# Kernel optimization log

Measured on AMD Instinct MI355X. Metric: run time of the kernel, lower is better.

The kernel has to match this reference:

```python
import jax, jax.numpy as jnp
import numpy as np

NUM_CLASSES = 80
INPUT_SHAPE = (416.0, 416.0)
ANCHORS_MASK0 = np.array([6, 7, 8])
CONF_THRES = 0.5
NMS_THRES = 0.4
IMAGE_SHAPE = (416.0, 416.0)
MAX_DET = 100          # fixed-size padded NMS output (jit-compatible)
CLASS_OFFSET = 4096.0  # class-aware box offset == independent per-class NMS
NEG = jnp.float32(-1e9)


def setup_inputs() -> dict:
    key = jax.random.key(0)
    inputs_1 = jax.random.normal(key, (32, 255, 52, 52), dtype=jnp.float32)
    anchors = jnp.array([[10, 13], [16, 30], [33, 23], [30, 61], [62, 45],
                         [59, 119], [116, 90], [156, 198], [373, 326]], dtype=jnp.float32)
    return {"inputs_1": inputs_1, "anchors": anchors}


def _decode(inputs_1, anchors):
    B, C, H, W = inputs_1.shape
    A = len(ANCHORS_MASK0)
    attrs = C // A  # 5 + num_classes
    # [B, A, H, W, attrs]
    pred = inputs_1.reshape(B, A, attrs, H, W).transpose(0, 1, 3, 4, 2)
    xy = jax.nn.sigmoid(pred[..., 0:2])
    wh = pred[..., 2:4]
    conf = jax.nn.sigmoid(pred[..., 4])
    cls = jax.nn.sigmoid(pred[..., 5:])
    stride_h = INPUT_SHAPE[0] / H
    stride_w = INPUT_SHAPE[1] / W
    anc = anchors[ANCHORS_MASK0] / jnp.array([stride_w, stride_h], jnp.float32)  # [A,2]
    gx = jnp.arange(W, dtype=jnp.float32)
    gy = jnp.arange(H, dtype=jnp.float32)
    bx = xy[..., 0] + gx[None, None, None, :]
    by = xy[..., 1] + gy[None, None, :, None]
    bw = jnp.exp(wh[..., 0]) * anc[:, 0][None, :, None, None]
    bh = jnp.exp(wh[..., 1]) * anc[:, 1][None, :, None, None]
    boxes = jnp.stack([bx, by, bw, bh], -1) / jnp.array([W, H, W, H], jnp.float32)
    return jnp.concatenate([boxes.reshape(B, -1, 4),
                            conf.reshape(B, -1, 1),
                            cls.reshape(B, -1, NUM_CLASSES)], axis=-1)  # [B, A*H*W, 5+C]


def _iou(box, boxes):
    lt = jnp.maximum(box[:2], boxes[:, :2])
    rb = jnp.minimum(box[2:], boxes[:, 2:])
    wh = jnp.clip(rb - lt, 0.0)
    inter = wh[:, 0] * wh[:, 1]
    a1 = (box[2] - box[0]) * (box[3] - box[1])
    a2 = (boxes[:, 2] - boxes[:, 0]) * (boxes[:, 3] - boxes[:, 1])
    return inter / (a1 + a2 - inter + 1e-9)


def _nms(pred0):
    # pred0: [N, 5+C] (image 0, matching torch code which only processes prediction[0])
    cx, cy, w, h = pred0[:, 0], pred0[:, 1], pred0[:, 2], pred0[:, 3]
    corners = jnp.stack([cx - w / 2, cy - h / 2, cx + w / 2, cy + h / 2], -1)  # [N,4]
    class_conf = jnp.max(pred0[:, 5:], axis=1)
    class_pred = jnp.argmax(pred0[:, 5:], axis=1)
    score = pred0[:, 4] * class_conf  # obj_conf * class_conf, same score nms() receives
    valid = score >= CONF_THRES
    # offsetting boxes by class id makes a single NMS pass equivalent to the per-class loop
    obox = corners + (class_pred.astype(jnp.float32) * CLASS_OFFSET)[:, None]
    s0 = jnp.where(valid, score, NEG)

    def step(scores, _):
        i = jnp.argmax(scores)
        flag = scores[i] > NEG / 2
        iou = _iou(obox[i], obox)
        new_scores = jnp.where(iou > NMS_THRES, NEG, scores).at[i].set(NEG)
        return new_scores, (i, flag)

    _, (idxs, flags) = jax.lax.scan(step, s0, None, length=MAX_DET)
    det = jnp.concatenate([
        corners[idxs],                                  # x1,y1,x2,y2
        pred0[idxs, 4:5],                               # obj conf
        class_conf[idxs][:, None],                      # class conf
        class_pred[idxs].astype(jnp.float32)[:, None],  # class id
    ], axis=1)  # [MAX_DET, 7]
    # yolo_correct_boxes: xywh -> yx min/max scaled to image_shape
    box_xy = (det[:, 0:2] + det[:, 2:4]) / 2.0
    box_wh = det[:, 2:4] - det[:, 0:2]
    box_yx = box_xy[:, ::-1]
    box_hw = box_wh[:, ::-1]
    mins = box_yx - box_hw / 2.0
    maxes = box_yx + box_hw / 2.0
    scale = jnp.array([IMAGE_SHAPE[0], IMAGE_SHAPE[1], IMAGE_SHAPE[0], IMAGE_SHAPE[1]], jnp.float32)
    boxes_corr = jnp.concatenate([mins, maxes], axis=1) * scale
    det = jnp.concatenate([boxes_corr, det[:, 4:]], axis=1)
    return det * flags[:, None].astype(jnp.float32)  # zero-padded rows where no detection


def reference(inputs_1, anchors):
    out = _decode(inputs_1, anchors)   # [B, 3*H*W, 5+num_classes]
    det = _nms(out[0])                 # [MAX_DET, 7], padded fixed-size NMS result
    return (out, det)
```

## Files before the change

kernel.cpp:

```cpp
#include <hip/hip_runtime.h>
#include <math.h>

constexpr int An = 3;
constexpr int Wd = 52;
constexpr int HWn = 2704;
constexpr int ATT = 85;
constexpr int CH = 208;
constexpr int PITCH = 209;
constexpr int CHUNKS = 13;
constexpr int DEC_BLOCKS = 96 * CHUNKS;
constexpr int NC = An * HWn;
constexpr int OUT_DEC = 32 * NC * ATT;
constexpr float NEGV = -1.0e9f;
constexpr int WS_SCORE_OFF = 65536;
constexpr int INFI = 0x7FFFFFFF;
constexpr size_t DEC_LDS = (size_t)ATT * PITCH * sizeof(float);

constexpr int L_BX1  = 16384;
constexpr int L_BY1  = 17408;
constexpr int L_BX2  = 18432;
constexpr int L_BY2  = 19456;
constexpr int L_BAR  = 20480;
constexpr int L_KEPT = 21504;
constexpr int L_DET  = 21904;
constexpr int L_WMIN = 22604;
constexpr int L_META = 22636;
constexpr size_t NMS_LDS = 22640u * sizeof(float);

__device__ __forceinline__ float sig_precise(float x) {
    return 1.0f / (1.0f + expf(-x));
}
__device__ __forceinline__ float sig_fast(float x) {
    return 1.0f / (1.0f + __expf(-x));
}

__global__ void __launch_bounds__(128)
yolo_prep(const float* __restrict__ in, const float* __restrict__ anc,
          float* __restrict__ ws)
{
    const int n = blockIdx.x * 128 + threadIdx.x;
    if (n >= NC) return;
    const int a   = n / HWn;
    const int pos = n - a * HWn;
    const float* p = in + (size_t)a * 85 * HWn + pos;

    const float tx = p[0];
    const float ty = p[HWn];
    const float tw = p[2 * HWn];
    const float th = p[3 * HWn];
    const float tc = p[4 * HWn];

    float m = -3.0e38f; int cp = 0;
    #pragma unroll
    for (int j0 = 0; j0 < 80; j0 += 16) {
        float v[16];
        #pragma unroll
        for (int u = 0; u < 16; ++u) v[u] = p[(size_t)(5 + j0 + u) * HWn];
        #pragma unroll
        for (int u = 0; u < 16; ++u) {
            if (v[u] > m) { m = v[u]; cp = j0 + u; }
        }
    }

    const float cc    = sig_precise(m);
    const float conf  = sig_precise(tc);
    const float score = __fmul_rn(conf, cc);
    const float aw = anc[(6 + a) * 2 + 0] * 0.125f;
    const float ah = anc[(6 + a) * 2 + 1] * 0.125f;
    const float cx = (sig_precise(tx) + (float)(pos % Wd)) / 52.0f;
    const float cy = (sig_precise(ty) + (float)(pos / Wd)) / 52.0f;
    const float bw = expf(tw) * aw / 52.0f;
    const float bh = expf(th) * ah / 52.0f;
    const float hw = __fmul_rn(bw, 0.5f);
    const float hh = __fmul_rn(bh, 0.5f);
    float4* w4 = (float4*)ws;
    w4[2 * n + 0] = make_float4(__fsub_rn(cx, hw), __fsub_rn(cy, hh),
                                __fadd_rn(cx, hw), __fadd_rn(cy, hh));
    w4[2 * n + 1] = make_float4(conf, cc, (float)cp, 0.0f);
    ws[WS_SCORE_OFF + n] = score;
}

__global__ void __launch_bounds__(1024)
yolo_nms(const float* __restrict__ ws, float* __restrict__ out)
{
    extern __shared__ float sm[];
    unsigned long long* keys = (unsigned long long*)sm;
    float* lx1 = sm + L_BX1;  float* ly1 = sm + L_BY1;
    float* lx2 = sm + L_BX2;  float* ly2 = sm + L_BY2;
    float* lar = sm + L_BAR;
    float4* keptv   = (float4*)(sm + L_KEPT);
    float* detstage = sm + L_DET;
    int*   wavemin  = (int*)(sm + L_WMIN);
    int*   meta     = (int*)(sm + L_META);
    const int tid  = threadIdx.x;
    const int lane = tid & 63;
    const int wv   = tid >> 6;

    if (tid == 0) meta[0] = 0;
    __syncthreads();

    const float* wscore = ws + WS_SCORE_OFF;
    for (int k = 0; k < 8; ++k) {
        const int n = tid + k * 1024;
        const float s = (n < NC) ? wscore[n] : NEGV;
        const bool valid = (s >= 0.5f);
        const unsigned long long mask = __ballot(valid);
        if (mask != 0ULL) {
            const int leader = __ffsll((long long)mask) - 1;
            int base = 0;
            if (lane == leader) base = atomicAdd(&meta[0], __popcll(mask));
            base = __shfl(base, leader);
            if (valid) {
                const int slot = base + __popcll(mask & ((1ULL << lane) - 1ULL));
                keys[slot] =
                    ((unsigned long long)(0xFFFFFFFFu - __float_as_uint(s)) << 32)
                    | (unsigned)n;
            }
        }
    }
    __syncthreads();
    const int V = meta[0];
    int P2 = 1; while (P2 < V) P2 <<= 1;
    for (int i = V + tid; i < P2; i += 1024) keys[i] = ~0ULL;
    __syncthreads();

    for (int k = 2; k <= P2; k <<= 1) {
        for (int j = k >> 1; j > 0; j >>= 1) {
            for (int idx = tid; idx < (P2 >> 1); idx += 1024) {
                const int i = ((idx & ~(j - 1)) << 1) | (idx & (j - 1));
                const int l = i | j;
                const unsigned long long a = keys[i], b = keys[l];
                const bool up = ((i & k) == 0);
                if (up ? (b < a) : (a < b)) { keys[i] = b; keys[l] = a; }
            }
            __syncthreads();
        }
    }

    const float4* w4 = (const float4*)ws;
    int nk = 0;
    for (int base = 0; base < V && nk < 100; base += 1024) {
        const int cidx = base + tid;
        bool alive = (cidx < V);
        float rx1 = 0, ry1 = 0, rx2 = 0, ry2 = 0, mconf = 0, mcc = 0, mcp = 0;
        float ox1 = 0, oy1 = 0, ox2 = 0, oy2 = 0, aC = 0;
        if (alive) {
            const int n = (int)(keys[cidx] & 0xFFFFFFFFu);
            const float4 bx = w4[2 * n], mt = w4[2 * n + 1];
            rx1 = bx.x; ry1 = bx.y; rx2 = bx.z; ry2 = bx.w;
            mconf = mt.x; mcc = mt.y; mcp = mt.z;
            const float off = __fmul_rn(mcp, 4096.0f);
            ox1 = __fadd_rn(rx1, off); oy1 = __fadd_rn(ry1, off);
            ox2 = __fadd_rn(rx2, off); oy2 = __fadd_rn(ry2, off);
            aC  = __fmul_rn(__fsub_rn(ox2, ox1), __fsub_rn(oy2, oy1));
            lx1[tid] = ox1; ly1[tid] = oy1; lx2[tid] = ox2; ly2[tid] = oy2;
            lar[tid] = aC;
            for (int t = 0; t < nk && alive; ++t) {
                const float4 kb = keptv[t];
                const float ltx = fmaxf(kb.x, ox1), lty = fmaxf(kb.y, oy1);
                const float rbx = fminf(kb.z, ox2), rby = fminf(kb.w, oy2);
                const float iw = fmaxf(__fsub_rn(rbx, ltx), 0.0f);
                const float ih = fmaxf(__fsub_rn(rby, lty), 0.0f);
                const float inter = __fmul_rn(iw, ih);
                const float aK = __fmul_rn(__fsub_rn(kb.z, kb.x), __fsub_rn(kb.w, kb.y));
                const float den = __fadd_rn(__fsub_rn(__fadd_rn(aK, aC), inter), 1e-9f);
                if (inter / den > 0.4f) alive = false;
            }
        }

        int it = 0;
        while (true) {
            const unsigned long long mb = __ballot(alive);
            if (lane == 0)
                wavemin[(it & 1) * 16 + wv] =
                    mb ? (wv * 64 + (__ffsll((long long)mb) - 1)) : INFI;
            __syncthreads();
            int win = INFI;
            #pragma unroll
            for (int w = 0; w < 16; ++w)
                win = min(win, wavemin[(it & 1) * 16 + w]);
            if (win == INFI) break;
            if (tid == win) {
                keptv[nk] = make_float4(ox1, oy1, ox2, oy2);
                float* dr = detstage + nk * 7;
                const float xm  = __fmul_rn(__fadd_rn(rx1, rx2), 0.5f);
                const float ym  = __fmul_rn(__fadd_rn(ry1, ry2), 0.5f);
                const float hw2 = __fmul_rn(__fsub_rn(rx2, rx1), 0.5f);
                const float hh2 = __fmul_rn(__fsub_rn(ry2, ry1), 0.5f);
                dr[0] = __fmul_rn(__fsub_rn(ym, hh2), 416.0f);
                dr[1] = __fmul_rn(__fsub_rn(xm, hw2), 416.0f);
                dr[2] = __fmul_rn(__fadd_rn(ym, hh2), 416.0f);
                dr[3] = __fmul_rn(__fadd_rn(xm, hw2), 416.0f);
                dr[4] = mconf; dr[5] = mcc; dr[6] = mcp;
                alive = false;
            }
            ++nk;
            if (nk == 100) break;
            if (alive) {
                const float wx1 = lx1[win], wy1 = ly1[win];
                const float wx2 = lx2[win], wy2 = ly2[win], aW = lar[win];
                const float ltx = fmaxf(wx1, ox1), lty = fmaxf(wy1, oy1);
                const float rbx = fminf(wx2, ox2), rby = fminf(wy2, oy2);
                const float iw = fmaxf(__fsub_rn(rbx, ltx), 0.0f);
                const float ih = fmaxf(__fsub_rn(rby, lty), 0.0f);
                const float inter = __fmul_rn(iw, ih);
                const float den = __fadd_rn(__fsub_rn(__fadd_rn(aW, aC), inter), 1e-9f);
                if (inter / den > 0.4f) alive = false;
            }
            ++it;
        }
        __syncthreads();
    }

    for (int i = tid; i < 100 * 7; i += 1024) {
        out[OUT_DEC + i] = (i < nk * 7) ? detstage[i] : 0.0f;
    }
}

__global__ void __launch_bounds__(1024)
yolo_decode(const float* __restrict__ in, const float* __restrict__ anc,
            float* __restrict__ out)
{
    extern __shared__ float smem[];
    const int tid = threadIdx.x;
    const int bi    = (int)blockIdx.x;
    const int chunk = bi % CHUNKS;
    const int ba    = bi / CHUNKS;
    const int a     = ba % An;
    const float anc_w = anc[(6 + a) * 2 + 0] * 0.125f;
    const float anc_h = anc[(6 + a) * 2 + 1] * 0.125f;
    const int pos0  = chunk * CH;
    const float* src = in + (size_t)ba * 85 * HWn + pos0;

    for (int i = tid; i < ATT * CH; i += 1024) {
        const int attr = i / CH;
        const int p    = i - attr * CH;
        const int pos  = pos0 + p;
        const float x  = src[(size_t)attr * HWn + p];
        float v;
        if (attr >= 4)      v = sig_fast(x);
        else if (attr == 0) v = (sig_fast(x) + (float)(pos % Wd)) / 52.0f;
        else if (attr == 1) v = (sig_fast(x) + (float)(pos / Wd)) / 52.0f;
        else if (attr == 2) v = __expf(x) * anc_w / 52.0f;
        else                v = __expf(x) * anc_h / 52.0f;
        smem[attr * PITCH + p] = v;
    }
    __syncthreads();

    float* dst = out + ((size_t)ba * HWn + pos0) * ATT;
    for (int f = tid; f < CH * ATT; f += 1024) {
        const int p    = f / ATT;
        const int attr = f - p * ATT;
        dst[f] = smem[attr * PITCH + p];
    }
}

extern "C" void kernel_launch(void* const* d_in, const int* in_sizes, int n_in,
                              void* d_out, int out_size, void* d_ws, size_t ws_size,
                              hipStream_t stream) {
    const float* in  = (const float*)d_in[0];
    const float* anc = (const float*)d_in[1];
    float* out = (float*)d_out;
    float* ws  = (float*)d_ws;

    hipLaunchKernelGGL(yolo_prep, dim3((NC + 127) / 128), dim3(128), 0, stream,
                       in, anc, ws);
    hipLaunchKernelGGL(yolo_nms, dim3(1), dim3(1024), NMS_LDS, stream, ws, out);
    hipLaunchKernelGGL(yolo_decode, dim3(DEC_BLOCKS), dim3(1024), DEC_LDS, stream,
                       in, anc, out);
}
```

Measured before the change: 290.3 us.

## Fuse NMS into decode kernel and replace sort with iterative argmax selection

Merges the single-block NMS kernel and the decode kernel into one launch: block 0 runs NMS while the remaining blocks run decode, so the serial NMS overlaps the bandwidth-bound decode. NMS drops the compaction and bitonic sort. Each candidate's score and offset box are held in registers, and each of up to 100 rounds does a block-wide argmax reduction and then suppresses boxes by IoU against the winner. This trades a sort for 100 reduction rounds with two barriers each, and block 0 may become the tail of the launch.

```diff
diff --git a/kernel.cpp b/kernel.cpp
--- a/kernel.cpp
+++ b/kernel.cpp
@@ -11,21 +11,8 @@
 constexpr int DEC_BLOCKS = 96 * CHUNKS;
 constexpr int NC = An * HWn;
 constexpr int OUT_DEC = 32 * NC * ATT;
-constexpr float NEGV = -1.0e9f;
 constexpr int WS_SCORE_OFF = 65536;
-constexpr int INFI = 0x7FFFFFFF;
 constexpr size_t DEC_LDS = (size_t)ATT * PITCH * sizeof(float);
-
-constexpr int L_BX1  = 16384;
-constexpr int L_BY1  = 17408;
-constexpr int L_BX2  = 18432;
-constexpr int L_BY2  = 19456;
-constexpr int L_BAR  = 20480;
-constexpr int L_KEPT = 21504;
-constexpr int L_DET  = 21904;
-constexpr int L_WMIN = 22604;
-constexpr int L_META = 22636;
-constexpr size_t NMS_LDS = 22640u * sizeof(float);
 
 __device__ __forceinline__ float sig_precise(float x) {
     return 1.0f / (1.0f + expf(-x));
@@ -81,177 +68,146 @@
 }
 
 __global__ void __launch_bounds__(1024)
-yolo_nms(const float* __restrict__ ws, float* __restrict__ out)
+yolo_fused(const float* __restrict__ in, const float* __restrict__ anc,
+           float* __restrict__ out, const float* __restrict__ ws)
 {
-    extern __shared__ float sm[];
-    unsigned long long* keys = (unsigned long long*)sm;
-    float* lx1 = sm + L_BX1;  float* ly1 = sm + L_BY1;
-    float* lx2 = sm + L_BX2;  float* ly2 = sm + L_BY2;
-    float* lar = sm + L_BAR;
-    float4* keptv   = (float4*)(sm + L_KEPT);
-    float* detstage = sm + L_DET;
-    int*   wavemin  = (int*)(sm + L_WMIN);
-    int*   meta     = (int*)(sm + L_META);
-    const int tid  = threadIdx.x;
-    const int lane = tid & 63;
-    const int wv   = tid >> 6;
-
-    if (tid == 0) meta[0] = 0;
-    __syncthreads();
-
+    extern __shared__ float dynsm[];
+    const int tid = threadIdx.x;
+
+    if (blockIdx.x != 0) {
+        const int bi    = (int)blockIdx.x - 1;
+        const int chunk = bi % CHUNKS;
+        const int ba    = bi / CHUNKS;
+        const int a     = ba % An;
+        const float anc_w = anc[(6 + a) * 2 + 0] * 0.125f;
+        const float anc_h = anc[(6 + a) * 2 + 1] * 0.125f;
+        const int pos0  = chunk * CH;
+        const float* src = in + (size_t)ba * 85 * HWn + pos0;
+
+        for (int i = tid; i < ATT * CH; i += 1024) {
+            const int attr = i / CH;
+            const int p    = i - attr * CH;
+            const int pos  = pos0 + p;
+            const float x  = src[(size_t)attr * HWn + p];
+            float v;
+            if (attr >= 4)      v = sig_fast(x);
+            else if (attr == 0) v = (sig_fast(x) + (float)(pos % Wd)) / 52.0f;
+            else if (attr == 1) v = (sig_fast(x) + (float)(pos / Wd)) / 52.0f;
+            else if (attr == 2) v = __expf(x) * anc_w / 52.0f;
+            else                v = __expf(x) * anc_h / 52.0f;
+            dynsm[attr * PITCH + p] = v;
+        }
+        __syncthreads();
+
+        float* dst = out + ((size_t)ba * HWn + pos0) * ATT;
+        for (int f = tid; f < CH * ATT; f += 1024) {
+            const int p    = f / ATT;
+            const int attr = f - p * ATT;
+            dst[f] = dynsm[attr * PITCH + p];
+        }
+        return;
+    }
+
+    unsigned long long* warr = (unsigned long long*)dynsm;
+    float* winslot  = dynsm + 64;
+    float* detstage = dynsm + 72;
+
+    float s[8], qx1[8], qy1[8], qx2[8], qy2[8];
+    const float4* w4 = (const float4*)ws;
     const float* wscore = ws + WS_SCORE_OFF;
+    #pragma unroll
     for (int k = 0; k < 8; ++k) {
-        const int n = tid + k * 1024;
-        const float s = (n < NC) ? wscore[n] : NEGV;
-        const bool valid = (s >= 0.5f);
-        const unsigned long long mask = __ballot(valid);
-        if (mask != 0ULL) {
-            const int leader = __ffsll((long long)mask) - 1;
-            int base = 0;
-            if (lane == leader) base = atomicAdd(&meta[0], __popcll(mask));
-            base = __shfl(base, leader);
-            if (valid) {
-                const int slot = base + __popcll(mask & ((1ULL << lane) - 1ULL));
-                keys[slot] =
-                    ((unsigned long long)(0xFFFFFFFFu - __float_as_uint(s)) << 32)
-                    | (unsigned)n;
+        const int n = k * 1024 + tid;
+        if (n < NC) {
+            const float sc = wscore[n];
+            s[k] = (sc >= 0.5f) ? sc : -1.0f;
+            const float4 b0 = w4[2 * n], b1 = w4[2 * n + 1];
+            const float off = __fmul_rn(b1.z, 4096.0f);
+            qx1[k] = __fadd_rn(b0.x, off);
+            qy1[k] = __fadd_rn(b0.y, off);
+            qx2[k] = __fadd_rn(b0.z, off);
+            qy2[k] = __fadd_rn(b0.w, off);
+        } else {
+            s[k] = -1.0f;
+            qx1[k] = qy1[k] = qx2[k] = qy2[k] = 0.0f;
+        }
+    }
+
+    int nk = 0;
+    for (int pick = 0; pick < 100; ++pick) {
+        float bs = 0.0f; int bn = 0;
+        #pragma unroll
+        for (int k = 0; k < 8; ++k) {
+            if (s[k] > bs) { bs = s[k]; bn = k * 1024 + tid; }
+        }
+        unsigned long long key = (bs > 0.0f)
+            ? (((unsigned long long)__float_as_uint(bs) << 32)
+               | (unsigned)(0xFFFFFFFFu - (unsigned)bn))
+            : 0ULL;
+        #pragma unroll
+        for (int o = 1; o < 64; o <<= 1) {
+            const unsigned long long other = __shfl_xor(key, o);
+            if (other > key) key = other;
+        }
+        if ((tid & 63) == 0) warr[(pick & 1) * 16 + (tid >> 6)] = key;
+        __syncthreads();
+        unsigned long long gk = 0ULL;
+        #pragma unroll
+        for (int w = 0; w < 16; ++w) {
+            const unsigned long long other = warr[(pick & 1) * 16 + w];
+            if (other > gk) gk = other;
+        }
+        if (gk == 0ULL) break;
+        const int nwin = (int)(0xFFFFFFFFu - (unsigned)(gk & 0xFFFFFFFFu));
+
+        if ((nwin & 1023) == tid) {
+            const int slot = nwin >> 10;
+            #pragma unroll
+            for (int k = 0; k < 8; ++k) {
+                if (k == slot) {
+                    winslot[0] = qx1[k]; winslot[1] = qy1[k];
+                    winslot[2] = qx2[k]; winslot[3] = qy2[k];
+                    winslot[4] = __fmul_rn(__fsub_rn(qx2[k], qx1[k]),
+                                           __fsub_rn(qy2[k], qy1[k]));
+                    s[k] = -1.0f;
+                }
             }
-        }
-    }
-    __syncthreads();
-    const int V = meta[0];
-    int P2 = 1; while (P2 < V) P2 <<= 1;
-    for (int i = V + tid; i < P2; i += 1024) keys[i] = ~0ULL;
-    __syncthreads();
-
-    for (int k = 2; k <= P2; k <<= 1) {
-        for (int j = k >> 1; j > 0; j >>= 1) {
-            for (int idx = tid; idx < (P2 >> 1); idx += 1024) {
-                const int i = ((idx & ~(j - 1)) << 1) | (idx & (j - 1));
-                const int l = i | j;
-                const unsigned long long a = keys[i], b = keys[l];
-                const bool up = ((i & k) == 0);
-                if (up ? (b < a) : (a < b)) { keys[i] = b; keys[l] = a; }
-            }
-            __syncthreads();
-        }
-    }
-
-    const float4* w4 = (const float4*)ws;
-    int nk = 0;
-    for (int base = 0; base < V && nk < 100; base += 1024) {
-        const int cidx = base + tid;
-        bool alive = (cidx < V);
-        float rx1 = 0, ry1 = 0, rx2 = 0, ry2 = 0, mconf = 0, mcc = 0, mcp = 0;
-        float ox1 = 0, oy1 = 0, ox2 = 0, oy2 = 0, aC = 0;
-        if (alive) {
-            const int n = (int)(keys[cidx] & 0xFFFFFFFFu);
-            const float4 bx = w4[2 * n], mt = w4[2 * n + 1];
-            rx1 = bx.x; ry1 = bx.y; rx2 = bx.z; ry2 = bx.w;
-            mconf = mt.x; mcc = mt.y; mcp = mt.z;
-            const float off = __fmul_rn(mcp, 4096.0f);
-            ox1 = __fadd_rn(rx1, off); oy1 = __fadd_rn(ry1, off);
-            ox2 = __fadd_rn(rx2, off); oy2 = __fadd_rn(ry2, off);
-            aC  = __fmul_rn(__fsub_rn(ox2, ox1), __fsub_rn(oy2, oy1));
-            lx1[tid] = ox1; ly1[tid] = oy1; lx2[tid] = ox2; ly2[tid] = oy2;
-            lar[tid] = aC;
-            for (int t = 0; t < nk && alive; ++t) {
-                const float4 kb = keptv[t];
-                const float ltx = fmaxf(kb.x, ox1), lty = fmaxf(kb.y, oy1);
-                const float rbx = fminf(kb.z, ox2), rby = fminf(kb.w, oy2);
+            const float4 b0 = w4[2 * nwin], b1 = w4[2 * nwin + 1];
+            float* dr = detstage + nk * 7;
+            const float xm  = __fmul_rn(__fadd_rn(b0.x, b0.z), 0.5f);
+            const float ym  = __fmul_rn(__fadd_rn(b0.y, b0.w), 0.5f);
+            const float hw2 = __fmul_rn(__fsub_rn(b0.z, b0.x), 0.5f);
+            const float hh2 = __fmul_rn(__fsub_rn(b0.w, b0.y), 0.5f);
+            dr[0] = __fmul_rn(__fsub_rn(ym, hh2), 416.0f);
+            dr[1] = __fmul_rn(__fsub_rn(xm, hw2), 416.0f);
+            dr[2] = __fmul_rn(__fadd_rn(ym, hh2), 416.0f);
+            dr[3] = __fmul_rn(__fadd_rn(xm, hw2), 416.0f);
+            dr[4] = b1.x; dr[5] = b1.y; dr[6] = b1.z;
+        }
+        __syncthreads();
+
+        const float wx1 = winslot[0], wy1 = winslot[1];
+        const float wx2 = winslot[2], wy2 = winslot[3], aW = winslot[4];
+        #pragma unroll
+        for (int k = 0; k < 8; ++k) {
+            if (s[k] >= 0.0f) {
+                const float ltx = fmaxf(wx1, qx1[k]), lty = fmaxf(wy1, qy1[k]);
+                const float rbx = fminf(wx2, qx2[k]), rby = fminf(wy2, qy2[k]);
                 const float iw = fmaxf(__fsub_rn(rbx, ltx), 0.0f);
                 const float ih = fmaxf(__fsub_rn(rby, lty), 0.0f);
                 const float inter = __fmul_rn(iw, ih);
-                const float aK = __fmul_rn(__fsub_rn(kb.z, kb.x), __fsub_rn(kb.w, kb.y));
-                const float den = __fadd_rn(__fsub_rn(__fadd_rn(aK, aC), inter), 1e-9f);
-                if (inter / den > 0.4f) alive = false;
+                const float aK = __fmul_rn(__fsub_rn(qx2[k], qx1[k]),
+                                           __fsub_rn(qy2[k], qy1[k]));
+                const float den = __fadd_rn(__fsub_rn(__fadd_rn(aW, aK), inter), 1e-9f);
+                if (inter / den > 0.4f) s[k] = -1.0f;
             }
         }
-
-        int it = 0;
-        while (true) {
-            const unsigned long long mb = __ballot(alive);
-            if (lane == 0)
-                wavemin[(it & 1) * 16 + wv] =
-                    mb ? (wv * 64 + (__ffsll((long long)mb) - 1)) : INFI;
-            __syncthreads();
-            int win = INFI;
-            #pragma unroll
-            for (int w = 0; w < 16; ++w)
-                win = min(win, wavemin[(it & 1) * 16 + w]);
-            if (win == INFI) break;
-            if (tid == win) {
-                keptv[nk] = make_float4(ox1, oy1, ox2, oy2);
-                float* dr = detstage + nk * 7;
-                const float xm  = __fmul_rn(__fadd_rn(rx1, rx2), 0.5f);
-                const float ym  = __fmul_rn(__fadd_rn(ry1, ry2), 0.5f);
-                const float hw2 = __fmul_rn(__fsub_rn(rx2, rx1), 0.5f);
-                const float hh2 = __fmul_rn(__fsub_rn(ry2, ry1), 0.5f);
-                dr[0] = __fmul_rn(__fsub_rn(ym, hh2), 416.0f);
-                dr[1] = __fmul_rn(__fsub_rn(xm, hw2), 416.0f);
-                dr[2] = __fmul_rn(__fadd_rn(ym, hh2), 416.0f);
-                dr[3] = __fmul_rn(__fadd_rn(xm, hw2), 416.0f);
-                dr[4] = mconf; dr[5] = mcc; dr[6] = mcp;
-                alive = false;
-            }
-            ++nk;
-            if (nk == 100) break;
-            if (alive) {
-                const float wx1 = lx1[win], wy1 = ly1[win];
-                const float wx2 = lx2[win], wy2 = ly2[win], aW = lar[win];
-                const float ltx = fmaxf(wx1, ox1), lty = fmaxf(wy1, oy1);
-                const float rbx = fminf(wx2, ox2), rby = fminf(wy2, oy2);
-                const float iw = fmaxf(__fsub_rn(rbx, ltx), 0.0f);
-                const float ih = fmaxf(__fsub_rn(rby, lty), 0.0f);
-                const float inter = __fmul_rn(iw, ih);
-                const float den = __fadd_rn(__fsub_rn(__fadd_rn(aW, aC), inter), 1e-9f);
-                if (inter / den > 0.4f) alive = false;
-            }
-            ++it;
-        }
-        __syncthreads();
-    }
+        ++nk;
+    }
+    __syncthreads();
 
     for (int i = tid; i < 100 * 7; i += 1024) {
         out[OUT_DEC + i] = (i < nk * 7) ? detstage[i] : 0.0f;
-    }
-}
-
-__global__ void __launch_bounds__(1024)
-yolo_decode(const float* __restrict__ in, const float* __restrict__ anc,
-            float* __restrict__ out)
-{
-    extern __shared__ float smem[];
-    const int tid = threadIdx.x;
-    const int bi    = (int)blockIdx.x;
-    const int chunk = bi % CHUNKS;
-    const int ba    = bi / CHUNKS;
-    const int a     = ba % An;
-    const float anc_w = anc[(6 + a) * 2 + 0] * 0.125f;
-    const float anc_h = anc[(6 + a) * 2 + 1] * 0.125f;
-    const int pos0  = chunk * CH;
-    const float* src = in + (size_t)ba * 85 * HWn + pos0;
-
-    for (int i = tid; i < ATT * CH; i += 1024) {
-        const int attr = i / CH;
-        const int p    = i - attr * CH;
-        const int pos  = pos0 + p;
-        const float x  = src[(size_t)attr * HWn + p];
-        float v;
-        if (attr >= 4)      v = sig_fast(x);
-        else if (attr == 0) v = (sig_fast(x) + (float)(pos % Wd)) / 52.0f;
-        else if (attr == 1) v = (sig_fast(x) + (float)(pos / Wd)) / 52.0f;
-        else if (attr == 2) v = __expf(x) * anc_w / 52.0f;
-        else                v = __expf(x) * anc_h / 52.0f;
-        smem[attr * PITCH + p] = v;
-    }
-    __syncthreads();
-
-    float* dst = out + ((size_t)ba * HWn + pos0) * ATT;
-    for (int f = tid; f < CH * ATT; f += 1024) {
-        const int p    = f / ATT;
-        const int attr = f - p * ATT;
-        dst[f] = smem[attr * PITCH + p];
     }
 }
 
@@ -265,7 +221,6 @@
 
     hipLaunchKernelGGL(yolo_prep, dim3((NC + 127) / 128), dim3(128), 0, stream,
                        in, anc, ws);
-    hipLaunchKernelGGL(yolo_nms, dim3(1), dim3(1024), NMS_LDS, stream, ws, out);
-    hipLaunchKernelGGL(yolo_decode, dim3(DEC_BLOCKS), dim3(1024), DEC_LDS, stream,
-                       in, anc, out);
-}
+    hipLaunchKernelGGL(yolo_fused, dim3(DEC_BLOCKS + 1), dim3(1024), DEC_LDS,
+                       stream, in, anc, out, ws);
+}
```

After: 510.7 us. 75.9% more time.
